# Kernel tuning notes

Hardware: AMD Instinct MI355X
Metric: run time of the kernel (lower is better)

Reference implementation:

```python
import jax, jax.numpy as jnp
import numpy as np

D_MODEL = 1024
N_HEADS = 16
D_HEAD = D_MODEL // N_HEADS
WINDOW = 64
SCALE = 1.0 / np.sqrt(D_HEAD)


def setup_inputs() -> dict:
    key = jax.random.key(0)
    k1, k2, k3 = jax.random.split(key, 3)
    B, N = 1, 4096
    x = jax.random.normal(k1, (B, N, D_MODEL), dtype=jnp.float32)
    # xavier-uniform-ish init for weights (scaled normal is fine for a numeric reference)
    w_qkv = jax.random.normal(k2, (3 * D_MODEL, D_MODEL), dtype=jnp.float32) * (1.0 / np.sqrt(D_MODEL))
    b_qkv = jnp.zeros((3 * D_MODEL,), dtype=jnp.float32)
    w_out = jax.random.normal(k3, (D_MODEL, D_MODEL), dtype=jnp.float32) * (1.0 / np.sqrt(D_MODEL))
    b_out = jnp.zeros((D_MODEL,), dtype=jnp.float32)
    return {"x": x, "w_qkv": w_qkv, "b_qkv": b_qkv, "w_out": w_out, "b_out": b_out}


def reference(x, w_qkv, b_qkv, w_out, b_out):
    B, N, D = x.shape
    # QKV projection (torch Linear: x @ W^T + b)
    qkv = x @ w_qkv.T + b_qkv                      # [B, N, 3D]
    qkv = qkv.reshape(B, N, 3, N_HEADS, D_HEAD)
    qkv = jnp.transpose(qkv, (2, 0, 3, 1, 4))       # [3, B, H, N, dh]
    q, k, v = qkv[0], qkv[1], qkv[2]
    # dense scores, masked to causal sliding window (faithful to original)
    scores = jnp.einsum('bhqd,bhkd->bhqk', q, k) * SCALE  # [B, H, N, N]
    qpos = jnp.arange(N)[:, None]
    kpos = jnp.arange(N)[None, :]
    diff = qpos - kpos
    mask = (diff >= 0) & (diff < WINDOW)            # [N, N]
    scores = jnp.where(mask[None, None, :, :], scores, -jnp.inf)
    attn = jax.nn.softmax(scores, axis=-1)          # every query has >=1 valid key (self)
    out = jnp.einsum('bhqk,bhkd->bhqd', attn, v)    # [B, H, N, dh]
    out = jnp.transpose(out, (0, 2, 1, 3)).reshape(B, N, D)
    out = out @ w_out.T + b_out
    return out
```

## Files before the change

### kernel.cpp

```cpp
#include <hip/hip_runtime.h>
#include <hip/hip_bf16.h>
#include <stdint.h>
#include <stddef.h>

#define NSEQ  4096
#define DM    1024
#define NHEAD 16
#define DHEAD 64
#define WIN   64

using short8 = __attribute__((ext_vector_type(8))) short;
using f32x4  = __attribute__((ext_vector_type(4))) float;

#define GLOBAL_AS __attribute__((address_space(1)))
#define LDS_AS    __attribute__((address_space(3)))

__device__ __forceinline__ unsigned short f2bf(float f) {
  union { float f; unsigned int u; } v; v.f = f;
  unsigned int r = v.u + 0x7FFFu + ((v.u >> 16) & 1u);
  return (unsigned short)(r >> 16);
}

__device__ __forceinline__ void gload_lds16(void* lds, const void* g) {
  __builtin_amdgcn_global_load_lds((const GLOBAL_AS unsigned int*)g,
                                   (LDS_AS unsigned int*)lds, 16, 0, 0);
}

#define NX4 1048576
#define NW4 786432
__global__ void cvt_all(const float* __restrict__ x,
                        const float* __restrict__ wqkv,
                        const float* __restrict__ wout,
                        unsigned short* __restrict__ dst) {
  int i = blockIdx.x * blockDim.x + threadIdx.x;
  float4 f;
  if (i < NX4)            f = ((const float4*)x)[i];
  else if (i < NX4 + NW4) f = ((const float4*)wqkv)[i - NX4];
  else                    f = ((const float4*)wout)[i - (NX4 + NW4)];
  ushort4 o;
  o.x = f2bf(f.x); o.y = f2bf(f.y); o.z = f2bf(f.z); o.w = f2bf(f.w);
  ((ushort4*)dst)[i] = o;
}

__global__ __launch_bounds__(512, 1)
void gemm_qkv(const unsigned short* __restrict__ A,
              const unsigned short* __restrict__ B,
              const float* __restrict__ bias,
              unsigned short* __restrict__ qo,
              unsigned short* __restrict__ ko,
              unsigned short* __restrict__ vo) {
  __shared__ short lds[57344];

  const int bm = blockIdx.x >> 4;
  const int bn = blockIdx.x & 15;
  const int m0 = bm << 8, n0 = bn * 192;
  const int tid = threadIdx.x, w = tid >> 6, l = tid & 63;
  const int wr = w >> 2, wc = w & 3;
  const int l15 = l & 15, l4 = l >> 4;
  const int srow = l >> 2;
  const int skel = ((l & 3) << 3) ^ ((l >= 32) << 4);
  const int roff = l15 * 32 + ((l4 * 8) ^ ((l15 >= 8) * 16));

  f32x4 acc[8][3] = {};

  auto stageA = [&](int j, int qm) {
    const int base = (j & 1) * 28672 + qm * 8192;
#pragma unroll
    for (int r = 0; r < 2; ++r) {
      const int c = r * 8 + w;
      gload_lds16(&lds[base + c * 512 + l * 8],
                  A + (size_t)(m0 + qm * 128 + (c >> 1) * 16 + srow) * 1024
                    + (j << 6) + (c & 1) * 32 + skel);
    }
  };
  auto stageB = [&](int j, int qk) {
    const int base = (j & 1) * 28672 + 16384 + qk * 6144;
    {
      const int c = w;
      gload_lds16(&lds[base + c * 512 + l * 8],
                  B + (size_t)(n0 + c * 16 + srow) * 1024
                    + (j << 6) + qk * 32 + skel);
    }
    {
      const int c = 8 + (w & 3);
      gload_lds16(&lds[base + c * 512 + l * 8],
                  B + (size_t)(n0 + c * 16 + srow) * 1024
                    + (j << 6) + qk * 32 + skel);
    }
  };

  stageA(0, 0); stageA(0, 1); stageB(0, 1); stageB(0, 0); stageB(1, 0);
  asm volatile("s_waitcnt vmcnt(2)" ::: "memory");
  __builtin_amdgcn_s_barrier();

  const int NT = 16;
  for (int j = 0; j < NT; ++j) {
    const int buf = (j & 1) * 28672;
    const short* Ah = &lds[buf + wr * 8192];
#pragma unroll
    for (int p = 0; p < 4; ++p) {
      const int qm = p & 1, qk = p >> 1;
      const short* Bh = &lds[buf + 16384 + qk * 6144];
      short8 af[4], bf[3];
#pragma unroll
      for (int i = 0; i < 4; ++i)
        af[i] = *(const short8*)&Ah[(qm * 4 + i) * 1024 + qk * 512 + roff];
#pragma unroll
      for (int ni = 0; ni < 3; ++ni)
        bf[ni] = *(const short8*)&Bh[(wc * 3 + ni) * 512 + roff];
      if (p == 0 && j + 1 < NT) { stageA(j + 1, 0); stageA(j + 1, 1); stageB(j + 1, 1); }
      if (p == 2 && j + 2 < NT) { stageB(j + 2, 0); }
      if (p == 3) {
        if (j + 2 < NT) asm volatile("s_waitcnt vmcnt(2)" ::: "memory");
        else            asm volatile("s_waitcnt vmcnt(0)" ::: "memory");
      } else {
        asm volatile("" ::: "memory");
      }
      __builtin_amdgcn_s_barrier();
      __builtin_amdgcn_s_setprio(1);
#pragma unroll
      for (int i = 0; i < 4; ++i)
#pragma unroll
        for (int ni = 0; ni < 3; ++ni)
          acc[qm * 4 + i][ni] = __builtin_amdgcn_mfma_f32_16x16x32_bf16(
              af[i], bf[ni], acc[qm * 4 + i][ni], 0, 0, 0);
      __builtin_amdgcn_s_setprio(0);
    }
  }

#pragma unroll
  for (int ni = 0; ni < 3; ++ni) {
    const int n  = n0 + wc * 48 + ni * 16 + l15;
    const float bv = bias[n];
    const int region = n >> 10;
#pragma unroll
    for (int mi = 0; mi < 8; ++mi) {
      const int mb = m0 + wr * 128 + mi * 16 + l4 * 4;
      if (region == 0) {
        const int h = (n >> 6) & 15, d = n & 63;
#pragma unroll
        for (int r = 0; r < 4; ++r)
          qo[((size_t)(h * NSEQ + mb + r)) * DHEAD + d] =
              f2bf((acc[mi][ni][r] + bv) * 0.125f);
      } else if (region == 1) {
        const int nn = n - 1024;
        const int h = nn >> 6, d = nn & 63;
#pragma unroll
        for (int r = 0; r < 4; ++r)
          ko[((size_t)(h * NSEQ + mb + r)) * DHEAD + d] =
              f2bf(acc[mi][ni][r] + bv);
      } else {
        const int nn = n - 2048;
        ushort4 pk;
        pk.x = f2bf(acc[mi][ni][0] + bv);
        pk.y = f2bf(acc[mi][ni][1] + bv);
        pk.z = f2bf(acc[mi][ni][2] + bv);
        pk.w = f2bf(acc[mi][ni][3] + bv);
        *(ushort4*)&vo[(size_t)nn * NSEQ + mb] = pk;
      }
    }
  }
}

__global__ __launch_bounds__(256)
void gemm_op(const unsigned short* __restrict__ A,
             const unsigned short* __restrict__ B,
             const float* __restrict__ bias,
             float* __restrict__ Cf) {
  __shared__ short lds[2][12288];

  const int wg = (blockIdx.x & 7) * 64 + (blockIdx.x >> 3);
  const int bm = wg >> 3;
  const int bn = wg & 7;
  const int m0 = bm << 6, n0 = bn << 7;
  const int tid = threadIdx.x, w = tid >> 6, l = tid & 63;
  const int wr = w >> 1, wc = w & 1;
  const int l15 = l & 15, l4 = l >> 4;
  const int srow = l >> 2;
  const int skel = ((l & 3) << 3) ^ ((l >= 32) << 4);
  const int roff = l15 * 32 + ((l4 * 8) ^ ((l15 >= 8) * 16));

  f32x4 acc[2][4] = {};
  const int NT = 16;

  auto stage = [&](int t) {
    const int buf = t & 1;
    const int kb  = t << 6;
#pragma unroll
    for (int r = 0; r < 2; ++r) {
      const int c = r * 4 + w;
      gload_lds16(&lds[buf][c * 512 + l * 8],
                  A + (size_t)(m0 + (c >> 1) * 16 + srow) * 1024
                    + kb + (c & 1) * 32 + skel);
    }
#pragma unroll
    for (int r = 0; r < 4; ++r) {
      const int c = r * 4 + w;
      gload_lds16(&lds[buf][4096 + c * 512 + l * 8],
                  B + (size_t)(n0 + (c >> 1) * 16 + srow) * 1024
                    + kb + (c & 1) * 32 + skel);
    }
  };

  stage(0);
  for (int t = 0; t < NT; ++t) {
    __syncthreads();
    if (t + 1 < NT) stage(t + 1);
    const short* Ab = &lds[t & 1][0];
    const short* Bb = &lds[t & 1][4096];
    short8 af[2][2], bf[4][2];
#pragma unroll
    for (int mi = 0; mi < 2; ++mi)
#pragma unroll
      for (int kk = 0; kk < 2; ++kk)
        af[mi][kk] = *(const short8*)&Ab[((wr * 2 + mi) * 2 + kk) * 512 + roff];
#pragma unroll
    for (int ni = 0; ni < 4; ++ni)
#pragma unroll
      for (int kk = 0; kk < 2; ++kk)
        bf[ni][kk] = *(const short8*)&Bb[((wc * 4 + ni) * 2 + kk) * 512 + roff];
    __builtin_amdgcn_s_setprio(1);
#pragma unroll
    for (int kk = 0; kk < 2; ++kk)
#pragma unroll
      for (int mi = 0; mi < 2; ++mi)
#pragma unroll
        for (int ni = 0; ni < 4; ++ni)
          acc[mi][ni] = __builtin_amdgcn_mfma_f32_16x16x32_bf16(
              af[mi][kk], bf[ni][kk], acc[mi][ni], 0, 0, 0);
    __builtin_amdgcn_s_setprio(0);
  }

#pragma unroll
  for (int ni = 0; ni < 4; ++ni) {
    const int n  = n0 + wc * 64 + ni * 16 + l15;
    const float bv = bias[n];
#pragma unroll
    for (int mi = 0; mi < 2; ++mi) {
      const int mb = m0 + wr * 32 + mi * 16 + l4 * 4;
#pragma unroll
      for (int r = 0; r < 4; ++r)
        Cf[(size_t)(mb + r) * DM + n] = acc[mi][ni][r] + bv;
    }
  }
}

__global__ __launch_bounds__(256)
void attn_kernel(const unsigned short* __restrict__ Qb,
                 const unsigned short* __restrict__ Kb,
                 const unsigned short* __restrict__ Vt,
                 unsigned short* __restrict__ att) {
  __shared__ short Pl[4][16][136];
  const int h  = blockIdx.x >> 6;
  const int q0 = (blockIdx.x & 63) << 6;
  const int w  = threadIdx.x >> 6;
  const int l  = threadIdx.x & 63;
  const int l15 = l & 15, l4 = l >> 4;
  const int qw = q0 + w * 16;
  const int tb = w & ~1;

  const unsigned short* Qh = Qb + (size_t)h * NSEQ * DHEAD;
  const unsigned short* Kh = Kb + (size_t)h * NSEQ * DHEAD;
  const unsigned short* Vh = Vt + (size_t)h * DHEAD * NSEQ;

  short8 aq[2];
  {
    const int qrow = qw + l15;
    aq[0] = *(const short8*)&Qh[(size_t)qrow * DHEAD + l4 * 8];
    aq[1] = *(const short8*)&Qh[(size_t)qrow * DHEAD + 32 + l4 * 8];
  }

  f32x4 s[6] = {};
#pragma unroll
  for (int tt = 0; tt < 6; ++tt) {
    int j  = q0 - 64 + (tb + tt) * 16 + l15;
    int jc = j < 0 ? 0 : j;
    short8 b0 = *(const short8*)&Kh[(size_t)jc * DHEAD + l4 * 8];
    short8 b1 = *(const short8*)&Kh[(size_t)jc * DHEAD + 32 + l4 * 8];
    s[tt] = __builtin_amdgcn_mfma_f32_16x16x32_bf16(aq[0], b0, s[tt], 0, 0, 0);
    s[tt] = __builtin_amdgcn_mfma_f32_16x16x32_bf16(aq[1], b1, s[tt], 0, 0, 0);
  }

  float rmax[4] = {-3e38f, -3e38f, -3e38f, -3e38f};
#pragma unroll
  for (int tt = 0; tt < 6; ++tt)
#pragma unroll
    for (int r = 0; r < 4; ++r) {
      const int i = qw + l4 * 4 + r;
      const int j = q0 - 64 + (tb + tt) * 16 + l15;
      const int diff = i - j;
      float sv = (j >= 0 && diff >= 0 && diff < WIN) ? s[tt][r] : -3e38f;
      s[tt][r] = sv;
      rmax[r] = fmaxf(rmax[r], sv);
    }
#pragma unroll
  for (int r = 0; r < 4; ++r)
#pragma unroll
    for (int m = 1; m < 16; m <<= 1)
      rmax[r] = fmaxf(rmax[r], __shfl_xor(rmax[r], m, 64));

  float rsum[4] = {0.f, 0.f, 0.f, 0.f};
#pragma unroll
  for (int tt = 0; tt < 6; ++tt)
#pragma unroll
    for (int r = 0; r < 4; ++r) {
      float p = __expf(s[tt][r] - rmax[r]);
      s[tt][r] = p;
      rsum[r] += p;
    }
#pragma unroll
  for (int r = 0; r < 4; ++r)
#pragma unroll
    for (int m = 1; m < 16; m <<= 1)
      rsum[r] += __shfl_xor(rsum[r], m, 64);

#pragma unroll
  for (int tt = 0; tt < 6; ++tt)
#pragma unroll
    for (int r = 0; r < 4; ++r)
      Pl[w][l4 * 4 + r][(tb + tt) * 16 + l15] = (short)f2bf(s[tt][r]);

  f32x4 o[4] = {};
#pragma unroll
  for (int kq = 0; kq < 3; ++kq) {
    const int ks = (w >> 1) + kq;
    short8 ap = *(const short8*)&Pl[w][l15][ks * 32 + l4 * 8];
    int jg = q0 - 64 + ks * 32 + l4 * 8;
    if (jg < 0) jg = 0;
#pragma unroll
    for (int dt = 0; dt < 4; ++dt) {
      const int d = dt * 16 + l15;
      short8 bv = *(const short8*)&Vh[(size_t)d * NSEQ + jg];
      o[dt] = __builtin_amdgcn_mfma_f32_16x16x32_bf16(ap, bv, o[dt], 0, 0, 0);
    }
  }

#pragma unroll
  for (int r = 0; r < 4; ++r) {
    const float rinv = 1.0f / rsum[r];
    const int m = qw + l4 * 4 + r;
#pragma unroll
    for (int dt = 0; dt < 4; ++dt)
      att[(size_t)m * DM + h * DHEAD + dt * 16 + l15] = f2bf(o[dt][r] * rinv);
  }
}

extern "C" void kernel_launch(void* const* d_in, const int* in_sizes, int n_in,
                              void* d_out, int out_size, void* d_ws, size_t ws_size,
                              hipStream_t stream) {
  const float* x    = (const float*)d_in[0];
  const float* wqkv = (const float*)d_in[1];
  const float* bqkv = (const float*)d_in[2];
  const float* wout = (const float*)d_in[3];
  const float* bout = (const float*)d_in[4];
  float* out = (float*)d_out;

  unsigned short* ws = (unsigned short*)d_ws;
  unsigned short* xb    = ws;
  unsigned short* wqkvb = xb    + (size_t)NSEQ * DM;
  unsigned short* woutb = wqkvb + (size_t)3 * DM * DM;
  unsigned short* qb    = woutb + (size_t)DM * DM;
  unsigned short* kb    = qb    + (size_t)NSEQ * DM;
  unsigned short* vtb   = kb    + (size_t)NSEQ * DM;
  unsigned short* attb  = vtb   + (size_t)NSEQ * DM;

  cvt_all<<<8192, 256, 0, stream>>>(x, wqkv, wout, xb);

  gemm_qkv<<<16 * 16, 512, 0, stream>>>(xb, wqkvb, bqkv, qb, kb, vtb);

  attn_kernel<<<NHEAD * (NSEQ / 64), 256, 0, stream>>>(qb, kb, vtb, attb);

  gemm_op<<<64 * 8, 256, 0, stream>>>(attb, woutb, bout, out);
}
```

Measured before the change: 80.18 us.

## Reshape QKV GEMM tile to 128x384 and restructure K-loop pipeline

Changes the QKV projection GEMM block tile from 256x192 to 128x384, so each wave holds a 64x96 output sub-tile (4x6 MFMA fragments). The K-step loop is simplified from four phases to two half-K phases with a reworked prefetch and wait schedule, and LDS use grows to hold the wider B tile. The goal is a different A/B reuse balance and fewer barriers per K step. The cost is more B traffic per block, a larger LDS footprint and more registers spent on B fragments.

```diff
diff --git a/kernel.cpp b/kernel.cpp
--- a/kernel.cpp
+++ b/kernel.cpp
@@ -49,11 +49,11 @@
               unsigned short* __restrict__ qo,
               unsigned short* __restrict__ ko,
               unsigned short* __restrict__ vo) {
-  __shared__ short lds[57344];
-
-  const int bm = blockIdx.x >> 4;
-  const int bn = blockIdx.x & 15;
-  const int m0 = bm << 8, n0 = bn * 192;
+  __shared__ short lds[65536];
+
+  const int bm = blockIdx.x >> 3;
+  const int bn = blockIdx.x & 7;
+  const int m0 = bm << 7, n0 = bn * 384;
   const int tid = threadIdx.x, w = tid >> 6, l = tid & 63;
   const int wr = w >> 2, wc = w & 3;
   const int l15 = l & 15, l4 = l >> 4;
@@ -61,81 +61,81 @@
   const int skel = ((l & 3) << 3) ^ ((l >= 32) << 4);
   const int roff = l15 * 32 + ((l4 * 8) ^ ((l15 >= 8) * 16));
 
-  f32x4 acc[8][3] = {};
-
-  auto stageA = [&](int j, int qm) {
-    const int base = (j & 1) * 28672 + qm * 8192;
+  f32x4 acc[4][6] = {};
+
+  auto stageA = [&](int j) {
+    const int base = (j & 1) * 32768;
 #pragma unroll
     for (int r = 0; r < 2; ++r) {
       const int c = r * 8 + w;
       gload_lds16(&lds[base + c * 512 + l * 8],
-                  A + (size_t)(m0 + qm * 128 + (c >> 1) * 16 + srow) * 1024
+                  A + (size_t)(m0 + (c >> 1) * 16 + srow) * 1024
                     + (j << 6) + (c & 1) * 32 + skel);
     }
   };
   auto stageB = [&](int j, int qk) {
-    const int base = (j & 1) * 28672 + 16384 + qk * 6144;
-    {
-      const int c = w;
+    const int base = (j & 1) * 32768 + 8192 + qk * 12288;
+#pragma unroll
+    for (int r = 0; r < 3; ++r) {
+      const int c = r * 8 + w;
       gload_lds16(&lds[base + c * 512 + l * 8],
                   B + (size_t)(n0 + c * 16 + srow) * 1024
                     + (j << 6) + qk * 32 + skel);
     }
-    {
-      const int c = 8 + (w & 3);
-      gload_lds16(&lds[base + c * 512 + l * 8],
-                  B + (size_t)(n0 + c * 16 + srow) * 1024
-                    + (j << 6) + qk * 32 + skel);
-    }
-  };
-
-  stageA(0, 0); stageA(0, 1); stageB(0, 1); stageB(0, 0); stageB(1, 0);
-  asm volatile("s_waitcnt vmcnt(2)" ::: "memory");
+  };
+
+  auto ldfrag = [&](short8* af, short8* bf, int buf, int qk) {
+    const short* Ah = &lds[buf];
+    const short* Bh = &lds[buf + 8192 + qk * 12288];
+#pragma unroll
+    for (int i = 0; i < 4; ++i)
+      af[i] = *(const short8*)&Ah[((wr * 4 + i) * 2 + qk) * 512 + roff];
+#pragma unroll
+    for (int ni = 0; ni < 6; ++ni)
+      bf[ni] = *(const short8*)&Bh[(wc * 6 + ni) * 512 + roff];
+  };
+  auto mfma24 = [&](const short8* af, const short8* bf) {
+    __builtin_amdgcn_s_setprio(1);
+#pragma unroll
+    for (int i = 0; i < 4; ++i)
+#pragma unroll
+      for (int ni = 0; ni < 6; ++ni)
+        acc[i][ni] = __builtin_amdgcn_mfma_f32_16x16x32_bf16(
+            af[i], bf[ni], acc[i][ni], 0, 0, 0);
+    __builtin_amdgcn_s_setprio(0);
+  };
+
+  stageA(0); stageB(0, 0); stageB(0, 1); stageB(1, 0);
+  asm volatile("s_waitcnt vmcnt(3)" ::: "memory");
   __builtin_amdgcn_s_barrier();
 
   const int NT = 16;
+  short8 af[4], bf[6];
   for (int j = 0; j < NT; ++j) {
-    const int buf = (j & 1) * 28672;
-    const short* Ah = &lds[buf + wr * 8192];
-#pragma unroll
-    for (int p = 0; p < 4; ++p) {
-      const int qm = p & 1, qk = p >> 1;
-      const short* Bh = &lds[buf + 16384 + qk * 6144];
-      short8 af[4], bf[3];
-#pragma unroll
-      for (int i = 0; i < 4; ++i)
-        af[i] = *(const short8*)&Ah[(qm * 4 + i) * 1024 + qk * 512 + roff];
-#pragma unroll
-      for (int ni = 0; ni < 3; ++ni)
-        bf[ni] = *(const short8*)&Bh[(wc * 3 + ni) * 512 + roff];
-      if (p == 0 && j + 1 < NT) { stageA(j + 1, 0); stageA(j + 1, 1); stageB(j + 1, 1); }
-      if (p == 2 && j + 2 < NT) { stageB(j + 2, 0); }
-      if (p == 3) {
-        if (j + 2 < NT) asm volatile("s_waitcnt vmcnt(2)" ::: "memory");
-        else            asm volatile("s_waitcnt vmcnt(0)" ::: "memory");
-      } else {
-        asm volatile("" ::: "memory");
-      }
-      __builtin_amdgcn_s_barrier();
-      __builtin_amdgcn_s_setprio(1);
-#pragma unroll
-      for (int i = 0; i < 4; ++i)
-#pragma unroll
-        for (int ni = 0; ni < 3; ++ni)
-          acc[qm * 4 + i][ni] = __builtin_amdgcn_mfma_f32_16x16x32_bf16(
-              af[i], bf[ni], acc[qm * 4 + i][ni], 0, 0, 0);
-      __builtin_amdgcn_s_setprio(0);
-    }
-  }
-
-#pragma unroll
-  for (int ni = 0; ni < 3; ++ni) {
-    const int n  = n0 + wc * 48 + ni * 16 + l15;
+    const int buf = (j & 1) * 32768;
+    ldfrag(af, bf, buf, 0);
+    if (j + 1 < NT) { stageA(j + 1); stageB(j + 1, 1); }
+    __builtin_amdgcn_s_barrier();
+    mfma24(af, bf);
+    ldfrag(af, bf, buf, 1);
+    if (j + 2 < NT) {
+      stageB(j + 2, 0);
+      asm volatile("s_waitcnt vmcnt(3)" ::: "memory");
+    } else if (j + 1 < NT) {
+      asm volatile("s_waitcnt vmcnt(0)" ::: "memory");
+    }
+    __builtin_amdgcn_s_barrier();
+    mfma24(af, bf);
+  }
+
+#pragma unroll
+  for (int ni = 0; ni < 6; ++ni) {
+    const int n  = n0 + wc * 96 + ni * 16 + l15;
     const float bv = bias[n];
     const int region = n >> 10;
 #pragma unroll
-    for (int mi = 0; mi < 8; ++mi) {
-      const int mb = m0 + wr * 128 + mi * 16 + l4 * 4;
+    for (int mi = 0; mi < 4; ++mi) {
+      const int mb = m0 + wr * 64 + mi * 16 + l4 * 4;
       if (region == 0) {
         const int h = (n >> 6) & 15, d = n & 63;
 #pragma unroll
@@ -366,7 +366,7 @@
 
   cvt_all<<<8192, 256, 0, stream>>>(x, wqkv, wout, xb);
 
-  gemm_qkv<<<16 * 16, 512, 0, stream>>>(xb, wqkvb, bqkv, qb, kb, vtb);
+  gemm_qkv<<<32 * 8, 512, 0, stream>>>(xb, wqkvb, bqkv, qb, kb, vtb);
 
   attn_kernel<<<NHEAD * (NSEQ / 64), 256, 0, stream>>>(qb, kb, vtb, attb);
 
```

After: 79.45 us. No clear change (-0.9%).
